# Kernel optimization log

Hardware: AMD Instinct MI355X
Metric: run time of the kernel (lower is better)

The kernel has to match this reference:

```python
import jax, jax.numpy as jnp
import numpy as np
from jax import lax

T, H, I, E = 1024, 1024, 512, 16          # tokens, hidden, moe_intermediate, n_routed_experts
TOP_K, N_GROUP, TOPK_GROUP = 4, 4, 2
N_SHARED = 2
I_SHARED = I * N_SHARED                    # shared-expert intermediate size
ROUTED_SCALE = 2.5


def setup_inputs() -> dict:
    key = jax.random.key(0)
    ks = jax.random.split(key, 9)
    s = lambda k, shape, fan: jax.random.normal(k, shape, jnp.float32) * (fan ** -0.5)
    return {
        "hidden_states": jax.random.normal(ks[0], (T, H), jnp.float32),
        "router_w": s(ks[1], (H, E), H),                 # gate: ReplicatedLinear(H, E)
        "e_bias": jax.random.normal(ks[2], (E,), jnp.float32) * 0.01,  # e_score_correction_bias
        "w_gate": s(ks[3], (E, H, I), H),                # routed experts gate_proj
        "w_up": s(ks[4], (E, H, I), H),                  # routed experts up_proj
        "w_down": s(ks[5], (E, I, H), I),                # routed experts down_proj
        "sw_gate": s(ks[6], (H, I_SHARED), H),           # shared experts gate_proj
        "sw_up": s(ks[7], (H, I_SHARED), H),             # shared experts up_proj
        "sw_down": s(ks[8], (I_SHARED, H), I_SHARED),    # shared experts down_proj
    }


def _grouped_topk_sigmoid(logits, e_bias):
    # DeepSeek-V3 'noaux_tc' grouped top-k with sigmoid scoring.
    scores = jax.nn.sigmoid(logits)                      # [T, E]
    sc = scores + e_bias                                 # biased scores for selection only
    g = sc.reshape(-1, N_GROUP, E // N_GROUP)
    group_scores = lax.top_k(g, 2)[0].sum(-1)            # [T, n_group]: sum of top-2 per group
    _, gidx = lax.top_k(group_scores, TOPK_GROUP)        # [T, topk_group]
    gmask = jax.nn.one_hot(gidx, N_GROUP, dtype=sc.dtype).sum(1)  # [T, n_group]
    emask = jnp.repeat(gmask, E // N_GROUP, axis=1)      # [T, E]
    masked = jnp.where(emask > 0, sc, 0.0)               # sigmoid scores are >=0
    _, tidx = lax.top_k(masked, TOP_K)                   # [T, top_k]
    w = jnp.take_along_axis(scores, tidx, axis=1)        # weights use UNbiased scores
    w = w / (w.sum(-1, keepdims=True) + 1e-20)           # norm_topk_prob=True
    # dense combine weights [T, E]
    combine = (jax.nn.one_hot(tidx, E, dtype=w.dtype) * w[..., None]).sum(1)
    return combine


def reference(hidden_states, router_w, e_bias, w_gate, w_up, w_down,
              sw_gate, sw_up, sw_down):
    x = hidden_states                                    # [T, H]
    logits = x @ router_w                                # [T, E]
    combine = _grouped_topk_sigmoid(logits, e_bias)      # [T, E]

    # routed experts: SiLU-gated MLP per expert, dense-over-experts reference
    gp = jnp.einsum('th,ehi->tei', x, w_gate)            # [T, E, I]
    up = jnp.einsum('th,ehi->tei', x, w_up)
    h = jax.nn.silu(gp) * up
    oe = jnp.einsum('tei,eih->teh', h, w_down)           # [T, E, H]
    routed = jnp.einsum('teh,te->th', oe, combine)       # [T, H]

    # shared experts MLP (reduce_results=False path), fp32 path scales routed only
    shared = (jax.nn.silu(x @ sw_gate) * (x @ sw_up)) @ sw_down  # [T, H]
    return routed * ROUTED_SCALE + shared
```

## Files before the change

kernel.cpp:

```cpp
#include <hip/hip_runtime.h>
#include <stdint.h>

#define T_TOK 1024
#define HDIM  1024
#define IDIM  512
#define NEXP  16
#define ISH   1024
#define MAXTILES 96
#define HSLOTS   5120

typedef _Float16 f16;
typedef __attribute__((ext_vector_type(8))) _Float16 f16x8;
typedef __attribute__((ext_vector_type(4))) _Float16 f16x4;
typedef __attribute__((ext_vector_type(4))) float    f32x4;

__device__ __forceinline__ void gld16(const void* g, void* l) {
  __builtin_amdgcn_global_load_lds(
      (__attribute__((address_space(1))) void*)(uintptr_t)g,
      (__attribute__((address_space(3))) void*)(uint32_t)(uintptr_t)l,
      16, 0, 0);
}

__device__ __forceinline__ f16x8 ldsfrag(const f16* buf, int row, int lch) {
  int phys = lch ^ (row & 7);
  return *(const f16x8*)(buf + row * 64 + phys * 8);
}

__global__ __launch_bounds__(256) void transpose_all(
    const float* __restrict__ wg, const float* __restrict__ wu, const float* __restrict__ wd,
    const float* __restrict__ sg, const float* __restrict__ su, const float* __restrict__ sd,
    f16* __restrict__ wgT, f16* __restrict__ wuT, f16* __restrict__ wdT,
    f16* __restrict__ sgT, f16* __restrict__ suT, f16* __restrict__ sdT) {
  int z = blockIdx.z;
  const float* src; f16* dst; int R, C;
  if (z < 16)       { src = wg + (size_t)z      * HDIM * IDIM; dst = wgT + (size_t)z      * HDIM * IDIM; R = HDIM; C = IDIM; }
  else if (z < 32)  { src = wu + (size_t)(z-16) * HDIM * IDIM; dst = wuT + (size_t)(z-16) * HDIM * IDIM; R = HDIM; C = IDIM; }
  else if (z < 48)  { src = wd + (size_t)(z-32) * IDIM * HDIM; dst = wdT + (size_t)(z-32) * IDIM * HDIM; R = IDIM; C = HDIM; }
  else if (z == 48) { src = sg; dst = sgT; R = HDIM; C = ISH; }
  else if (z == 49) { src = su; dst = suT; R = HDIM; C = ISH; }
  else              { src = sd; dst = sdT; R = ISH;  C = HDIM; }
  int c0 = blockIdx.x * 64, r0 = blockIdx.y * 64;
  if (c0 >= C || r0 >= R) return;
  __shared__ float tile[64][65];
  int t = threadIdx.x;
  int lr = t >> 4, c4 = (t & 15) * 4;
#pragma unroll
  for (int pass = 0; pass < 4; pass++) {
    int r = pass * 16 + lr;
    float4 v = *(const float4*)(src + (size_t)(r0 + r) * C + (c0 + c4));
    tile[r][c4 + 0] = v.x; tile[r][c4 + 1] = v.y;
    tile[r][c4 + 2] = v.z; tile[r][c4 + 3] = v.w;
  }
  __syncthreads();
  int oc = t >> 2, or0 = (t & 3) * 16;
  f16x8 v0, v1;
#pragma unroll
  for (int i = 0; i < 8; i++) {
    v0[i] = (f16)tile[or0 + i][oc];
    v1[i] = (f16)tile[or0 + 8 + i][oc];
  }
  f16* dp = dst + (size_t)(c0 + oc) * R + r0 + or0;
  *(f16x8*)dp = v0;
  *(f16x8*)(dp + 8) = v1;
}

__global__ __launch_bounds__(256) void router_kernel(
    const float* __restrict__ x, const float* __restrict__ rw, const float* __restrict__ ebias,
    f16* __restrict__ xh, int* __restrict__ topk_i, float* __restrict__ topk_w) {
  int wave = threadIdx.x >> 6, l = threadIdx.x & 63;
  int t = blockIdx.x * 4 + wave;
  float acc[16];
#pragma unroll
  for (int e = 0; e < 16; e++) acc[e] = 0.f;
#pragma unroll
  for (int i = 0; i < 4; i++) {
    int k = i * 256 + l * 4;
    float4 xv = *(const float4*)(x + (size_t)t * HDIM + k);
    f16x4 h = { (f16)xv.x, (f16)xv.y, (f16)xv.z, (f16)xv.w };
    *(f16x4*)(xh + (size_t)t * HDIM + k) = h;
    const float* xp = &xv.x;
#pragma unroll
    for (int j = 0; j < 4; j++) {
      float xj = xp[j];
      const float4* w4 = (const float4*)(rw + (size_t)(k + j) * 16);
#pragma unroll
      for (int q = 0; q < 4; q++) {
        float4 w = w4[q];
        acc[q*4+0] += xj * w.x; acc[q*4+1] += xj * w.y;
        acc[q*4+2] += xj * w.z; acc[q*4+3] += xj * w.w;
      }
    }
  }
#pragma unroll
  for (int off = 32; off >= 1; off >>= 1)
#pragma unroll
    for (int e = 0; e < 16; e++) acc[e] += __shfl_xor(acc[e], off, 64);

  if (l == 0) {
    float s[16], sc[16];
#pragma unroll
    for (int e = 0; e < 16; e++) {
      s[e] = 1.f / (1.f + __expf(-acc[e]));
      sc[e] = s[e] + ebias[e];
    }
    float gs[4];
#pragma unroll
    for (int g = 0; g < 4; g++) {
      float a = -1e30f, b = -1e30f;
#pragma unroll
      for (int j = 0; j < 4; j++) {
        float v = sc[g*4 + j];
        if (v > a) { b = a; a = v; } else if (v > b) { b = v; }
      }
      gs[g] = a + b;
    }
    int g1 = 0;
    for (int g = 1; g < 4; g++) if (gs[g] > gs[g1]) g1 = g;
    int g2 = -1;
    for (int g = 0; g < 4; g++) if (g != g1 && (g2 < 0 || gs[g] > gs[g2])) g2 = g;
    float masked[16];
#pragma unroll
    for (int e = 0; e < 16; e++) {
      int g = e >> 2;
      masked[e] = (g == g1 || g == g2) ? sc[e] : 0.0f;
    }
    int idx[4]; float wv[4]; float denom = 1e-20f;
#pragma unroll
    for (int j = 0; j < 4; j++) {
      int best = 0; float bv = masked[0];
      for (int e = 1; e < 16; e++) if (masked[e] > bv) { bv = masked[e]; best = e; }
      idx[j] = best; wv[j] = s[best]; denom += s[best];
      masked[best] = -1e30f;
    }
#pragma unroll
    for (int j = 0; j < 4; j++) {
      topk_i[t * 4 + j] = idx[j];
      topk_w[t * 4 + j] = wv[j] / denom * 2.5f;
    }
  }
}

__global__ __launch_bounds__(1024) void scatter_kernel(
    const int* __restrict__ tki,
    int* __restrict__ tok, int* __restrict__ slotmap,
    int* __restrict__ tile_e, int* __restrict__ tile_srow,
    int* __restrict__ tile_hb, int* __restrict__ ntl) {
  __shared__ int lcnt[NEXP], lpos[NEXP], lbase[NEXP];
  int t = threadIdx.x;
  if (t < NEXP) { lcnt[t] = 0; lpos[t] = 0; }
  __syncthreads();
  int idx[4];
#pragma unroll
  for (int j = 0; j < 4; j++) idx[j] = tki[t*4+j];
#pragma unroll
  for (int j = 0; j < 4; j++) atomicAdd(&lcnt[idx[j]], 1);
  __syncthreads();
  if (t == 0) {
    int total = 0, slots = 0;
    for (int e = 0; e < NEXP; e++) {
      int c = lcnt[e], nt = (c + 63) >> 6;
      lbase[e] = slots;
      for (int j = 0; j < nt; j++) {
        tile_e[total] = e; tile_srow[total] = j * 64; tile_hb[total] = slots + j * 64; total++;
      }
      slots += nt * 64;
    }
    ntl[0] = total;
  }
  __syncthreads();
#pragma unroll
  for (int j = 0; j < 4; j++) {
    int slot = atomicAdd(&lpos[idx[j]], 1);
    tok[idx[j] * T_TOK + slot] = t;
    slotmap[t * 4 + j] = lbase[idx[j]] + slot;
  }
  __syncthreads();
  int e = t >> 6, s = t & 63;
  int c = lcnt[e];
  int top = ((c + 63) >> 6) << 6;
  if (c + s < top) tok[e * T_TOK + c + s] = 0;
}

__device__ __forceinline__ f32x4 mfma16(f16x8 a, f16x8 b, f32x4 c) {
  return __builtin_amdgcn_mfma_f32_16x16x32_f16(a, b, c, 0, 0, 0);
}

__global__ __launch_bounds__(256) void gu_all(
    const f16* __restrict__ xh,
    const f16* __restrict__ sgT, const f16* __restrict__ suT, f16* __restrict__ hsh,
    const f16* __restrict__ wgT, const f16* __restrict__ wuT, f16* __restrict__ hbuf,
    const int* __restrict__ tile_e, const int* __restrict__ tile_srow,
    const int* __restrict__ tile_hb, const int* __restrict__ ntl,
    const int* __restrict__ tok) {
  int b = blockIdx.x;
  const f16 *Bg, *Bu; f16* Hdst;
  int e = 0, srow = 0, mbase, n0, N;
  bool gather = (b >= 256);
  if (!gather) {
    Bg = sgT; Bu = suT; Hdst = hsh; N = ISH;
    n0 = (b & 15) * 64; mbase = (b >> 4) * 64;
  } else {
    int rb = b - 256, by = rb >> 3;
    if (by >= ntl[0]) return;
    e = tile_e[by]; srow = tile_srow[by]; mbase = tile_hb[by];
    size_t bo = (size_t)e * IDIM * HDIM;
    Bg = wgT + bo; Bu = wuT + bo; Hdst = hbuf; N = IDIM;
    n0 = (rb & 7) * 64;
  }
  const int K = HDIM;

  __shared__ f16 As[64 * 64], Bgs[64 * 64], Bus[64 * 64];

  int tid = threadIdx.x, lane = tid & 63, wave = tid >> 6;
  int quad = lane >> 4, l15 = lane & 15;
  int r = lane >> 3, p = lane & 7;

  const f16* gb[6]; f16* lb[6];
#pragma unroll
  for (int jj = 0; jj < 6; jj++) {
    int j = wave * 6 + jj;
    int buf = j >> 3, i = j & 7;
    int row = i * 8 + r;
    int kcol = (p ^ r) << 3;
    if (buf == 0) {
      int grow = gather ? tok[e * T_TOK + srow + row] : (mbase + row);
      gb[jj] = xh + (size_t)grow * K + kcol;       lb[jj] = (f16*)As + (i << 9);
    } else if (buf == 1) {
      gb[jj] = Bg + (size_t)(n0 + row) * K + kcol; lb[jj] = (f16*)Bgs + (i << 9);
    } else {
      gb[jj] = Bu + (size_t)(n0 + row) * K + kcol; lb[jj] = (f16*)Bus + (i << 9);
    }
  }

  int wr = wave >> 1, wc = wave & 1;
  int ar0 = 32 * wr + l15, br0 = 32 * wc + l15;
  f32x4 zero = {0.f, 0.f, 0.f, 0.f};
  f32x4 aG[2][2] = {{zero, zero}, {zero, zero}};
  f32x4 aU[2][2] = {{zero, zero}, {zero, zero}};

  for (int kt = 0; kt < K; kt += 64) {
    __syncthreads();
#pragma unroll
    for (int jj = 0; jj < 6; jj++) gld16(gb[jj] + kt, lb[jj]);
    __syncthreads();
#pragma unroll
    for (int ks = 0; ks < 2; ks++) {
      int lch = (ks << 2) + quad;
      f16x8 a0 = ldsfrag(As,  ar0,      lch);
      f16x8 a1 = ldsfrag(As,  ar0 + 16, lch);
      f16x8 g0 = ldsfrag(Bgs, br0,      lch);
      f16x8 g1 = ldsfrag(Bgs, br0 + 16, lch);
      f16x8 u0 = ldsfrag(Bus, br0,      lch);
      f16x8 u1 = ldsfrag(Bus, br0 + 16, lch);
      aG[0][0] = mfma16(a0, g0, aG[0][0]); aG[0][1] = mfma16(a0, g1, aG[0][1]);
      aG[1][0] = mfma16(a1, g0, aG[1][0]); aG[1][1] = mfma16(a1, g1, aG[1][1]);
      aU[0][0] = mfma16(a0, u0, aU[0][0]); aU[0][1] = mfma16(a0, u1, aU[0][1]);
      aU[1][0] = mfma16(a1, u0, aU[1][0]); aU[1][1] = mfma16(a1, u1, aU[1][1]);
    }
  }
#pragma unroll
  for (int mi = 0; mi < 2; mi++)
#pragma unroll
    for (int ni = 0; ni < 2; ni++)
#pragma unroll
      for (int rg = 0; rg < 4; rg++) {
        int m = 32 * wr + 16 * mi + (quad << 2) + rg;
        int n = n0 + 32 * wc + 16 * ni + l15;
        float g = aG[mi][ni][rg], u = aU[mi][ni][rg];
        float val = (g / (1.f + __expf(-g))) * u;
        Hdst[(size_t)(mbase + m) * N + n] = (f16)val;
      }
}

__global__ __launch_bounds__(256) void down_all(
    const f16* __restrict__ hsh, const f16* __restrict__ sdT,
    const f16* __restrict__ hbuf, const f16* __restrict__ wdT,
    float* __restrict__ out, f16* __restrict__ odown,
    const int* __restrict__ tile_e, const int* __restrict__ tile_srow,
    const int* __restrict__ tile_hb, const int* __restrict__ ntl) {
  int b = blockIdx.x;
  bool routed = (b >= 256);
  const f16 *A, *B; int K, abase, n0, e = 0;
  if (!routed) {
    A = hsh; B = sdT; K = ISH;
    abase = (b >> 4) * 64; n0 = (b & 15) * 64;
  } else {
    int rb = b - 256, by = rb >> 4;
    if (by >= ntl[0]) return;
    e = tile_e[by]; abase = tile_hb[by];
    A = hbuf; B = wdT + (size_t)e * HDIM * IDIM; K = IDIM;
    n0 = (rb & 15) * 64;
  }

  __shared__ f16 As[64 * 64], Bs[64 * 64];

  int tid = threadIdx.x, lane = tid & 63, wave = tid >> 6;
  int quad = lane >> 4, l15 = lane & 15;
  int r = lane >> 3, p = lane & 7;

  const f16* gb[4]; f16* lb[4];
#pragma unroll
  for (int jj = 0; jj < 4; jj++) {
    int j = wave * 4 + jj;
    int buf = j >> 3, i = j & 7;
    int row = i * 8 + r;
    int kcol = (p ^ r) << 3;
    if (buf == 0) { gb[jj] = A + (size_t)(abase + row) * K + kcol; lb[jj] = (f16*)As + (i << 9); }
    else          { gb[jj] = B + (size_t)(n0 + row) * K + kcol;    lb[jj] = (f16*)Bs + (i << 9); }
  }

  int wr = wave >> 1, wc = wave & 1;
  int ar0 = 32 * wr + l15, br0 = 32 * wc + l15;
  f32x4 zero = {0.f, 0.f, 0.f, 0.f};
  f32x4 ac[2][2] = {{zero, zero}, {zero, zero}};

  for (int kt = 0; kt < K; kt += 64) {
    __syncthreads();
#pragma unroll
    for (int jj = 0; jj < 4; jj++) gld16(gb[jj] + kt, lb[jj]);
    __syncthreads();
#pragma unroll
    for (int ks = 0; ks < 2; ks++) {
      int lch = (ks << 2) + quad;
      f16x8 a0 = ldsfrag(As, ar0,      lch);
      f16x8 a1 = ldsfrag(As, ar0 + 16, lch);
      f16x8 b0 = ldsfrag(Bs, br0,      lch);
      f16x8 b1 = ldsfrag(Bs, br0 + 16, lch);
      ac[0][0] = mfma16(a0, b0, ac[0][0]); ac[0][1] = mfma16(a0, b1, ac[0][1]);
      ac[1][0] = mfma16(a1, b0, ac[1][0]); ac[1][1] = mfma16(a1, b1, ac[1][1]);
    }
  }
#pragma unroll
  for (int mi = 0; mi < 2; mi++)
#pragma unroll
    for (int ni = 0; ni < 2; ni++)
#pragma unroll
      for (int rg = 0; rg < 4; rg++) {
        int m = 32 * wr + 16 * mi + (quad << 2) + rg;
        int n = n0 + 32 * wc + 16 * ni + l15;
        if (routed) odown[(size_t)(abase + m) * HDIM + n] = (f16)ac[mi][ni][rg];
        else        out  [(size_t)(abase + m) * HDIM + n] = ac[mi][ni][rg];
      }
}

__global__ __launch_bounds__(256) void combine_kernel(
    const f16* __restrict__ odown, const int* __restrict__ slotmap,
    const float* __restrict__ tkw, float* __restrict__ out) {
  int t = blockIdx.x;
  __shared__ int ss[4]; __shared__ float sw[4];
  if (threadIdx.x < 4) {
    ss[threadIdx.x] = slotmap[t * 4 + threadIdx.x];
    sw[threadIdx.x] = tkw[t * 4 + threadIdx.x];
  }
  __syncthreads();
  int h = threadIdx.x * 4;
  float4 acc = *(const float4*)(out + (size_t)t * HDIM + h);
#pragma unroll
  for (int j = 0; j < 4; j++) {
    f16x4 v = *(const f16x4*)(odown + (size_t)ss[j] * HDIM + h);
    float wj = sw[j];
    acc.x += wj * (float)v[0]; acc.y += wj * (float)v[1];
    acc.z += wj * (float)v[2]; acc.w += wj * (float)v[3];
  }
  *(float4*)(out + (size_t)t * HDIM + h) = acc;
}

extern "C" void kernel_launch(void* const* d_in, const int* in_sizes, int n_in,
                              void* d_out, int out_size, void* d_ws, size_t ws_size,
                              hipStream_t stream) {
  const float* x  = (const float*)d_in[0];
  const float* rw = (const float*)d_in[1];
  const float* eb = (const float*)d_in[2];
  const float* wg = (const float*)d_in[3];
  const float* wu = (const float*)d_in[4];
  const float* wd = (const float*)d_in[5];
  const float* sg = (const float*)d_in[6];
  const float* su = (const float*)d_in[7];
  const float* sd = (const float*)d_in[8];
  float* out = (float*)d_out;
  (void)in_sizes; (void)n_in; (void)out_size; (void)ws_size;

  char* w = (char*)d_ws;
  size_t off = 0;
  auto alloc = [&](size_t b) { void* p = w + off; off = (off + b + 255) & ~(size_t)255; return p; };

  f16* xh   = (f16*)alloc((size_t)T_TOK * HDIM * 2);
  f16* wgT  = (f16*)alloc((size_t)NEXP * IDIM * HDIM * 2);
  f16* wuT  = (f16*)alloc((size_t)NEXP * IDIM * HDIM * 2);
  f16* wdT  = (f16*)alloc((size_t)NEXP * HDIM * IDIM * 2);
  f16* sgT  = (f16*)alloc((size_t)ISH * HDIM * 2);
  f16* suT  = (f16*)alloc((size_t)ISH * HDIM * 2);
  f16* sdT  = (f16*)alloc((size_t)HDIM * ISH * 2);
  f16* hbuf = (f16*)alloc((size_t)HSLOTS * IDIM * 2);
  f16* hsh  = (f16*)alloc((size_t)T_TOK * ISH * 2);
  int* topk_i = (int*)alloc((size_t)T_TOK * 4 * 4);
  float* topk_w = (float*)alloc((size_t)T_TOK * 4 * 4);
  int* tok  = (int*)alloc((size_t)NEXP * T_TOK * 4);
  int* slotmap = (int*)alloc((size_t)T_TOK * 4 * 4);
  int* tile_e    = (int*)alloc(MAXTILES * 4);
  int* tile_srow = (int*)alloc(MAXTILES * 4);
  int* tile_hb   = (int*)alloc(MAXTILES * 4);
  int* ntl       = (int*)alloc(16);
  f16* odown = (f16*)wgT;

  transpose_all<<<dim3(16, 16, 51), 256, 0, stream>>>(wg, wu, wd, sg, su, sd,
                                                      wgT, wuT, wdT, sgT, suT, sdT);
  router_kernel<<<T_TOK / 4, 256, 0, stream>>>(x, rw, eb, xh, topk_i, topk_w);
  scatter_kernel<<<1, 1024, 0, stream>>>(topk_i, tok, slotmap,
                                         tile_e, tile_srow, tile_hb, ntl);
  gu_all<<<256 + (MAXTILES - 16) * 8, 256, 0, stream>>>(
      xh, sgT, suT, hsh, wgT, wuT, hbuf, tile_e, tile_srow, tile_hb, ntl, tok);
  down_all<<<256 + (MAXTILES - 16) * 16, 256, 0, stream>>>(
      hsh, sdT, hbuf, wdT, out, odown, tile_e, tile_srow, tile_hb, ntl);
  combine_kernel<<<T_TOK, 256, 0, stream>>>(odown, slotmap, topk_w, out);
}
```

Measured before the change: 229.1 us.

## Enlarge GEMM tiles to 128 rows and batch transpose tiles per block

Raises the M tile of the gate/up kernel to 128 rows and the down kernel to 128x128, so each wave holds more accumulators and reuses every LDS fragment across more MFMAs. Expert routing is padded to 128-row tiles to match, with the scatter and slot layout changed accordingly. The weight transpose now walks four 64x64 tiles per block over a flat grid. More reuse and fewer blocks come at the price of more padding waste on small experts, higher register and LDS use per block, and fewer blocks for load balance.

Measured after the change: 230.0 us. Within noise of the previous version (+0.4%).

```diff
diff --git a/kernel.cpp b/kernel.cpp
--- a/kernel.cpp
+++ b/kernel.cpp
@@ -6,8 +6,8 @@
 #define IDIM  512
 #define NEXP  16
 #define ISH   1024
-#define MAXTILES 96
-#define HSLOTS   5120
+#define MAXT128  48
+#define HSLOTS   6144
 
 typedef _Float16 f16;
 typedef __attribute__((ext_vector_type(8))) _Float16 f16x8;
@@ -31,37 +31,44 @@
     const float* __restrict__ sg, const float* __restrict__ su, const float* __restrict__ sd,
     f16* __restrict__ wgT, f16* __restrict__ wuT, f16* __restrict__ wdT,
     f16* __restrict__ sgT, f16* __restrict__ suT, f16* __restrict__ sdT) {
-  int z = blockIdx.z;
-  const float* src; f16* dst; int R, C;
-  if (z < 16)       { src = wg + (size_t)z      * HDIM * IDIM; dst = wgT + (size_t)z      * HDIM * IDIM; R = HDIM; C = IDIM; }
-  else if (z < 32)  { src = wu + (size_t)(z-16) * HDIM * IDIM; dst = wuT + (size_t)(z-16) * HDIM * IDIM; R = HDIM; C = IDIM; }
-  else if (z < 48)  { src = wd + (size_t)(z-32) * IDIM * HDIM; dst = wdT + (size_t)(z-32) * IDIM * HDIM; R = IDIM; C = HDIM; }
-  else if (z == 48) { src = sg; dst = sgT; R = HDIM; C = ISH; }
-  else if (z == 49) { src = su; dst = suT; R = HDIM; C = ISH; }
-  else              { src = sd; dst = sdT; R = ISH;  C = HDIM; }
-  int c0 = blockIdx.x * 64, r0 = blockIdx.y * 64;
-  if (c0 >= C || r0 >= R) return;
   __shared__ float tile[64][65];
   int t = threadIdx.x;
-  int lr = t >> 4, c4 = (t & 15) * 4;
-#pragma unroll
-  for (int pass = 0; pass < 4; pass++) {
-    int r = pass * 16 + lr;
-    float4 v = *(const float4*)(src + (size_t)(r0 + r) * C + (c0 + c4));
-    tile[r][c4 + 0] = v.x; tile[r][c4 + 1] = v.y;
-    tile[r][c4 + 2] = v.z; tile[r][c4 + 3] = v.w;
-  }
-  __syncthreads();
-  int oc = t >> 2, or0 = (t & 3) * 16;
-  f16x8 v0, v1;
-#pragma unroll
-  for (int i = 0; i < 8; i++) {
-    v0[i] = (f16)tile[or0 + i][oc];
-    v1[i] = (f16)tile[or0 + 8 + i][oc];
-  }
-  f16* dp = dst + (size_t)(c0 + oc) * R + r0 + or0;
-  *(f16x8*)dp = v0;
-  *(f16x8*)(dp + 8) = v1;
+#pragma unroll
+  for (int it = 0; it < 4; it++) {
+    int ti = blockIdx.x * 4 + it;
+    const float* src; f16* dst; int R, C, within, clog;
+    if (ti < 2048)      { int e2 = ti >> 7; within = ti & 127; R = HDIM; C = IDIM; clog = 3;
+                          src = wg + (size_t)e2 * HDIM * IDIM; dst = wgT + (size_t)e2 * HDIM * IDIM; }
+    else if (ti < 4096) { int u = ti - 2048; int e2 = u >> 7; within = u & 127; R = HDIM; C = IDIM; clog = 3;
+                          src = wu + (size_t)e2 * HDIM * IDIM; dst = wuT + (size_t)e2 * HDIM * IDIM; }
+    else if (ti < 6144) { int u = ti - 4096; int e2 = u >> 7; within = u & 127; R = IDIM; C = HDIM; clog = 4;
+                          src = wd + (size_t)e2 * IDIM * HDIM; dst = wdT + (size_t)e2 * IDIM * HDIM; }
+    else                { int u = ti - 6144; int which = u >> 8; within = u & 255; R = HDIM; C = ISH; clog = 4;
+                          src = which == 0 ? sg : (which == 1 ? su : sd);
+                          dst = which == 0 ? sgT : (which == 1 ? suT : sdT); }
+    int r0 = (within >> clog) * 64, c0 = (within & ((1 << clog) - 1)) * 64;
+
+    if (it) __syncthreads();
+    int lr = t >> 4, c4 = (t & 15) * 4;
+#pragma unroll
+    for (int pass = 0; pass < 4; pass++) {
+      int r = pass * 16 + lr;
+      float4 v = *(const float4*)(src + (size_t)(r0 + r) * C + (c0 + c4));
+      tile[r][c4 + 0] = v.x; tile[r][c4 + 1] = v.y;
+      tile[r][c4 + 2] = v.z; tile[r][c4 + 3] = v.w;
+    }
+    __syncthreads();
+    int oc = t >> 2, or0 = (t & 3) * 16;
+    f16x8 v0, v1;
+#pragma unroll
+    for (int i = 0; i < 8; i++) {
+      v0[i] = (f16)tile[or0 + i][oc];
+      v1[i] = (f16)tile[or0 + 8 + i][oc];
+    }
+    f16* dp = dst + (size_t)(c0 + oc) * R + r0 + or0;
+    *(f16x8*)dp = v0;
+    *(f16x8*)(dp + 8) = v1;
+  }
 }
 
 __global__ __launch_bounds__(256) void router_kernel(
@@ -158,12 +165,12 @@
   if (t == 0) {
     int total = 0, slots = 0;
     for (int e = 0; e < NEXP; e++) {
-      int c = lcnt[e], nt = (c + 63) >> 6;
+      int c = lcnt[e], nt = (c + 127) >> 7;
       lbase[e] = slots;
       for (int j = 0; j < nt; j++) {
-        tile_e[total] = e; tile_srow[total] = j * 64; tile_hb[total] = slots + j * 64; total++;
-      }
-      slots += nt * 64;
+        tile_e[total] = e; tile_srow[total] = j * 128; tile_hb[total] = slots + j * 128; total++;
+      }
+      slots += nt * 128;
     }
     ntl[0] = total;
   }
@@ -177,8 +184,8 @@
   __syncthreads();
   int e = t >> 6, s = t & 63;
   int c = lcnt[e];
-  int top = ((c + 63) >> 6) << 6;
-  if (c + s < top) tok[e * T_TOK + c + s] = 0;
+  int top = ((c + 127) >> 7) << 7;
+  for (int s2 = c + s; s2 < top; s2 += 64) tok[e * T_TOK + s2] = 0;
 }
 
 __device__ __forceinline__ f32x4 mfma16(f16x8 a, f16x8 b, f32x4 c) {
@@ -195,12 +202,12 @@
   int b = blockIdx.x;
   const f16 *Bg, *Bu; f16* Hdst;
   int e = 0, srow = 0, mbase, n0, N;
-  bool gather = (b >= 256);
+  bool gather = (b >= 128);
   if (!gather) {
     Bg = sgT; Bu = suT; Hdst = hsh; N = ISH;
-    n0 = (b & 15) * 64; mbase = (b >> 4) * 64;
+    mbase = (b >> 4) * 128; n0 = (b & 15) * 64;
   } else {
-    int rb = b - 256, by = rb >> 3;
+    int rb = b - 128, by = rb >> 3;
     if (by >= ntl[0]) return;
     e = tile_e[by]; srow = tile_srow[by]; mbase = tile_hb[by];
     size_t bo = (size_t)e * IDIM * HDIM;
@@ -209,62 +216,70 @@
   }
   const int K = HDIM;
 
-  __shared__ f16 As[64 * 64], Bgs[64 * 64], Bus[64 * 64];
+  __shared__ f16 As[128 * 64], Bgs[64 * 64], Bus[64 * 64];
 
   int tid = threadIdx.x, lane = tid & 63, wave = tid >> 6;
   int quad = lane >> 4, l15 = lane & 15;
   int r = lane >> 3, p = lane & 7;
 
-  const f16* gb[6]; f16* lb[6];
-#pragma unroll
-  for (int jj = 0; jj < 6; jj++) {
-    int j = wave * 6 + jj;
-    int buf = j >> 3, i = j & 7;
-    int row = i * 8 + r;
+  const f16* gb[8]; f16* lb[8];
+#pragma unroll
+  for (int jj = 0; jj < 8; jj++) {
+    int j = wave * 8 + jj;
     int kcol = (p ^ r) << 3;
-    if (buf == 0) {
+    if (j < 16) {
+      int row = j * 8 + r;
       int grow = gather ? tok[e * T_TOK + srow + row] : (mbase + row);
-      gb[jj] = xh + (size_t)grow * K + kcol;       lb[jj] = (f16*)As + (i << 9);
-    } else if (buf == 1) {
+      gb[jj] = xh + (size_t)grow * K + kcol;       lb[jj] = (f16*)As + (j << 9);
+    } else if (j < 24) {
+      int i = j - 16, row = i * 8 + r;
       gb[jj] = Bg + (size_t)(n0 + row) * K + kcol; lb[jj] = (f16*)Bgs + (i << 9);
     } else {
+      int i = j - 24, row = i * 8 + r;
       gb[jj] = Bu + (size_t)(n0 + row) * K + kcol; lb[jj] = (f16*)Bus + (i << 9);
     }
   }
 
   int wr = wave >> 1, wc = wave & 1;
-  int ar0 = 32 * wr + l15, br0 = 32 * wc + l15;
   f32x4 zero = {0.f, 0.f, 0.f, 0.f};
-  f32x4 aG[2][2] = {{zero, zero}, {zero, zero}};
-  f32x4 aU[2][2] = {{zero, zero}, {zero, zero}};
+  f32x4 aG[4][2], aU[4][2];
+#pragma unroll
+  for (int mi = 0; mi < 4; mi++)
+#pragma unroll
+    for (int ni = 0; ni < 2; ni++) { aG[mi][ni] = zero; aU[mi][ni] = zero; }
 
   for (int kt = 0; kt < K; kt += 64) {
     __syncthreads();
 #pragma unroll
-    for (int jj = 0; jj < 6; jj++) gld16(gb[jj] + kt, lb[jj]);
+    for (int jj = 0; jj < 8; jj++) gld16(gb[jj] + kt, lb[jj]);
     __syncthreads();
 #pragma unroll
     for (int ks = 0; ks < 2; ks++) {
       int lch = (ks << 2) + quad;
-      f16x8 a0 = ldsfrag(As,  ar0,      lch);
-      f16x8 a1 = ldsfrag(As,  ar0 + 16, lch);
-      f16x8 g0 = ldsfrag(Bgs, br0,      lch);
-      f16x8 g1 = ldsfrag(Bgs, br0 + 16, lch);
-      f16x8 u0 = ldsfrag(Bus, br0,      lch);
-      f16x8 u1 = ldsfrag(Bus, br0 + 16, lch);
-      aG[0][0] = mfma16(a0, g0, aG[0][0]); aG[0][1] = mfma16(a0, g1, aG[0][1]);
-      aG[1][0] = mfma16(a1, g0, aG[1][0]); aG[1][1] = mfma16(a1, g1, aG[1][1]);
-      aU[0][0] = mfma16(a0, u0, aU[0][0]); aU[0][1] = mfma16(a0, u1, aU[0][1]);
-      aU[1][0] = mfma16(a1, u0, aU[1][0]); aU[1][1] = mfma16(a1, u1, aU[1][1]);
-    }
-  }
-#pragma unroll
-  for (int mi = 0; mi < 2; mi++)
+      f16x8 a[4], g[2], u[2];
+#pragma unroll
+      for (int mi = 0; mi < 4; mi++) a[mi] = ldsfrag(As, 64 * wr + 16 * mi + l15, lch);
+#pragma unroll
+      for (int ni = 0; ni < 2; ni++) {
+        g[ni] = ldsfrag(Bgs, 32 * wc + 16 * ni + l15, lch);
+        u[ni] = ldsfrag(Bus, 32 * wc + 16 * ni + l15, lch);
+      }
+#pragma unroll
+      for (int mi = 0; mi < 4; mi++)
+#pragma unroll
+        for (int ni = 0; ni < 2; ni++) {
+          aG[mi][ni] = mfma16(a[mi], g[ni], aG[mi][ni]);
+          aU[mi][ni] = mfma16(a[mi], u[ni], aU[mi][ni]);
+        }
+    }
+  }
+#pragma unroll
+  for (int mi = 0; mi < 4; mi++)
 #pragma unroll
     for (int ni = 0; ni < 2; ni++)
 #pragma unroll
       for (int rg = 0; rg < 4; rg++) {
-        int m = 32 * wr + 16 * mi + (quad << 2) + rg;
+        int m = 64 * wr + 16 * mi + (quad << 2) + rg;
         int n = n0 + 32 * wc + 16 * ni + l15;
         float g = aG[mi][ni][rg], u = aU[mi][ni][rg];
         float val = (g / (1.f + __expf(-g))) * u;
@@ -276,68 +291,78 @@
     const f16* __restrict__ hsh, const f16* __restrict__ sdT,
     const f16* __restrict__ hbuf, const f16* __restrict__ wdT,
     float* __restrict__ out, f16* __restrict__ odown,
-    const int* __restrict__ tile_e, const int* __restrict__ tile_srow,
-    const int* __restrict__ tile_hb, const int* __restrict__ ntl) {
+    const int* __restrict__ tile_hb, const int* __restrict__ tile_e,
+    const int* __restrict__ ntl) {
   int b = blockIdx.x;
-  bool routed = (b >= 256);
-  const f16 *A, *B; int K, abase, n0, e = 0;
+  bool routed = (b >= 64);
+  const f16 *A, *B; int K, abase, n0;
   if (!routed) {
     A = hsh; B = sdT; K = ISH;
-    abase = (b >> 4) * 64; n0 = (b & 15) * 64;
+    abase = (b >> 3) * 128; n0 = (b & 7) * 128;
   } else {
-    int rb = b - 256, by = rb >> 4;
+    int rb = b - 64, by = rb >> 3;
     if (by >= ntl[0]) return;
-    e = tile_e[by]; abase = tile_hb[by];
-    A = hbuf; B = wdT + (size_t)e * HDIM * IDIM; K = IDIM;
-    n0 = (rb & 15) * 64;
-  }
-
-  __shared__ f16 As[64 * 64], Bs[64 * 64];
+    abase = tile_hb[by];
+    A = hbuf; B = wdT + (size_t)tile_e[by] * HDIM * IDIM; K = IDIM;
+    n0 = (rb & 7) * 128;
+  }
+
+  __shared__ f16 As[128 * 64], Bs[128 * 64];
 
   int tid = threadIdx.x, lane = tid & 63, wave = tid >> 6;
   int quad = lane >> 4, l15 = lane & 15;
   int r = lane >> 3, p = lane & 7;
 
-  const f16* gb[4]; f16* lb[4];
-#pragma unroll
-  for (int jj = 0; jj < 4; jj++) {
-    int j = wave * 4 + jj;
-    int buf = j >> 3, i = j & 7;
-    int row = i * 8 + r;
+  const f16* gb[8]; f16* lb[8];
+#pragma unroll
+  for (int jj = 0; jj < 8; jj++) {
+    int j = wave * 8 + jj;
     int kcol = (p ^ r) << 3;
-    if (buf == 0) { gb[jj] = A + (size_t)(abase + row) * K + kcol; lb[jj] = (f16*)As + (i << 9); }
-    else          { gb[jj] = B + (size_t)(n0 + row) * K + kcol;    lb[jj] = (f16*)Bs + (i << 9); }
+    if (j < 16) {
+      int row = j * 8 + r;
+      gb[jj] = A + (size_t)(abase + row) * K + kcol; lb[jj] = (f16*)As + (j << 9);
+    } else {
+      int i = j - 16, row = i * 8 + r;
+      gb[jj] = B + (size_t)(n0 + row) * K + kcol;    lb[jj] = (f16*)Bs + (i << 9);
+    }
   }
 
   int wr = wave >> 1, wc = wave & 1;
-  int ar0 = 32 * wr + l15, br0 = 32 * wc + l15;
   f32x4 zero = {0.f, 0.f, 0.f, 0.f};
-  f32x4 ac[2][2] = {{zero, zero}, {zero, zero}};
+  f32x4 ac[4][4];
+#pragma unroll
+  for (int mi = 0; mi < 4; mi++)
+#pragma unroll
+    for (int ni = 0; ni < 4; ni++) ac[mi][ni] = zero;
 
   for (int kt = 0; kt < K; kt += 64) {
     __syncthreads();
 #pragma unroll
-    for (int jj = 0; jj < 4; jj++) gld16(gb[jj] + kt, lb[jj]);
+    for (int jj = 0; jj < 8; jj++) gld16(gb[jj] + kt, lb[jj]);
     __syncthreads();
 #pragma unroll
     for (int ks = 0; ks < 2; ks++) {
       int lch = (ks << 2) + quad;
-      f16x8 a0 = ldsfrag(As, ar0,      lch);
-      f16x8 a1 = ldsfrag(As, ar0 + 16, lch);
-      f16x8 b0 = ldsfrag(Bs, br0,      lch);
-      f16x8 b1 = ldsfrag(Bs, br0 + 16, lch);
-      ac[0][0] = mfma16(a0, b0, ac[0][0]); ac[0][1] = mfma16(a0, b1, ac[0][1]);
-      ac[1][0] = mfma16(a1, b0, ac[1][0]); ac[1][1] = mfma16(a1, b1, ac[1][1]);
-    }
-  }
-#pragma unroll
-  for (int mi = 0; mi < 2; mi++)
-#pragma unroll
-    for (int ni = 0; ni < 2; ni++)
+      f16x8 a[4], bb[4];
+#pragma unroll
+      for (int mi = 0; mi < 4; mi++) a[mi] = ldsfrag(As, 64 * wr + 16 * mi + l15, lch);
+#pragma unroll
+      for (int ni = 0; ni < 4; ni++) bb[ni] = ldsfrag(Bs, 64 * wc + 16 * ni + l15, lch);
+#pragma unroll
+      for (int mi = 0; mi < 4; mi++)
+#pragma unroll
+        for (int ni = 0; ni < 4; ni++)
+          ac[mi][ni] = mfma16(a[mi], bb[ni], ac[mi][ni]);
+    }
+  }
+#pragma unroll
+  for (int mi = 0; mi < 4; mi++)
+#pragma unroll
+    for (int ni = 0; ni < 4; ni++)
 #pragma unroll
       for (int rg = 0; rg < 4; rg++) {
-        int m = 32 * wr + 16 * mi + (quad << 2) + rg;
-        int n = n0 + 32 * wc + 16 * ni + l15;
+        int m = 64 * wr + 16 * mi + (quad << 2) + rg;
+        int n = n0 + 64 * wc + 16 * ni + l15;
         if (routed) odown[(size_t)(abase + m) * HDIM + n] = (f16)ac[mi][ni][rg];
         else        out  [(size_t)(abase + m) * HDIM + n] = ac[mi][ni][rg];
       }
@@ -397,20 +422,20 @@
   float* topk_w = (float*)alloc((size_t)T_TOK * 4 * 4);
   int* tok  = (int*)alloc((size_t)NEXP * T_TOK * 4);
   int* slotmap = (int*)alloc((size_t)T_TOK * 4 * 4);
-  int* tile_e    = (int*)alloc(MAXTILES * 4);
-  int* tile_srow = (int*)alloc(MAXTILES * 4);
-  int* tile_hb   = (int*)alloc(MAXTILES * 4);
+  int* tile_e    = (int*)alloc(MAXT128 * 4);
+  int* tile_srow = (int*)alloc(MAXT128 * 4);
+  int* tile_hb   = (int*)alloc(MAXT128 * 4);
   int* ntl       = (int*)alloc(16);
   f16* odown = (f16*)wgT;
 
-  transpose_all<<<dim3(16, 16, 51), 256, 0, stream>>>(wg, wu, wd, sg, su, sd,
-                                                      wgT, wuT, wdT, sgT, suT, sdT);
+  transpose_all<<<1728, 256, 0, stream>>>(wg, wu, wd, sg, su, sd,
+                                          wgT, wuT, wdT, sgT, suT, sdT);
   router_kernel<<<T_TOK / 4, 256, 0, stream>>>(x, rw, eb, xh, topk_i, topk_w);
   scatter_kernel<<<1, 1024, 0, stream>>>(topk_i, tok, slotmap,
                                          tile_e, tile_srow, tile_hb, ntl);
-  gu_all<<<256 + (MAXTILES - 16) * 8, 256, 0, stream>>>(
+  gu_all<<<128 + MAXT128 * 8, 256, 0, stream>>>(
       xh, sgT, suT, hsh, wgT, wuT, hbuf, tile_e, tile_srow, tile_hb, ntl, tok);
-  down_all<<<256 + (MAXTILES - 16) * 16, 256, 0, stream>>>(
-      hsh, sdT, hbuf, wdT, out, odown, tile_e, tile_srow, tile_hb, ntl);
+  down_all<<<64 + MAXT128 * 8, 256, 0, stream>>>(
+      hsh, sdT, hbuf, wdT, out, odown, tile_hb, tile_e, ntl);
   combine_kernel<<<T_TOK, 256, 0, stream>>>(odown, slotmap, topk_w, out);
 }
```
